# Performance work log

Hardware: AMD Instinct MI355X
Metric: run time of the kernel (lower is better)

## Reference

```python
import jax, jax.numpy as jnp
import numpy as np

LUT_VALS = np.array([-1.0, -0.5, -0.333333, -0.2, -0.142857, -0.090909, -0.076923,
                     0.0, 0.076923, 0.090909, 0.142857, 0.2, 0.333333, 0.5, 1.0],
                    dtype=np.float32)

B, S, IN, OUT = 4, 2048, 2048, 8192


def setup_inputs() -> dict:
    key = jax.random.key(0)
    kx, ki = jax.random.split(key)
    x = jax.random.normal(kx, (B, S, IN), dtype=jnp.float32)
    # uint8 LUT indices into the 15-entry primal grid (stored int32 for jax indexing)
    grid_indices = jax.random.randint(ki, (OUT, IN), 0, 15, dtype=jnp.int32)
    scale = jnp.float32(1.0)
    lut = jnp.asarray(LUT_VALS)
    return {"x": x, "grid_indices": grid_indices, "scale": scale, "lut": lut}


def reference(x, grid_indices, scale, lut):
    # Dequantize: gather LUT values by index, then scalar scale (GhostQuantFunction.forward)
    weights = lut[grid_indices] * scale          # [OUT, IN] fp32
    # F.linear(x, weights): y = x @ W^T
    return jnp.einsum('bsi,oi->bso', x, weights)
```

## Files before the change

### kernel.cpp

```cpp
#include <hip/hip_runtime.h>
#include <cstdint>

typedef short bf16x8 __attribute__((ext_vector_type(8)));
typedef unsigned short u16x8 __attribute__((ext_vector_type(8)));
typedef float f32x4 __attribute__((ext_vector_type(4)));
typedef __attribute__((address_space(3))) uint32_t lds_u32;
typedef const __attribute__((address_space(1))) uint32_t gbl_u32;

__device__ __forceinline__ unsigned short f2bf(float f) {
  union { float f; uint32_t u; } c; c.f = f;
  uint32_t u = c.u;
  return (unsigned short)((u + 0x7fffu + ((u >> 16) & 1u)) >> 16);
}

__global__ void cvt_x_kernel(const float* __restrict__ x,
                             unsigned short* __restrict__ y, long n) {
  long t = (long)blockIdx.x * blockDim.x + threadIdx.x;
  long base = t * 8;
  if (base >= n) return;
  const float4* p = (const float4*)(x + base);
  float4 f0 = p[0], f1 = p[1];
  u16x8 v;
  v[0] = f2bf(f0.x); v[1] = f2bf(f0.y); v[2] = f2bf(f0.z); v[3] = f2bf(f0.w);
  v[4] = f2bf(f1.x); v[5] = f2bf(f1.y); v[6] = f2bf(f1.z); v[7] = f2bf(f1.w);
  *(u16x8*)(y + base) = v;
}

__global__ void dequant_kernel(const int* __restrict__ idx,
                               const float* __restrict__ lut,
                               const float* __restrict__ scale,
                               unsigned short* __restrict__ w, long n) {
  __shared__ unsigned short slut[16];
  if (threadIdx.x < 15) slut[threadIdx.x] = f2bf(lut[threadIdx.x] * scale[0]);
  __syncthreads();
  long t = (long)blockIdx.x * blockDim.x + threadIdx.x;
  long base = t * 8;
  if (base >= n) return;
  const int4* p = (const int4*)(idx + base);
  int4 i0 = p[0], i1 = p[1];
  u16x8 v;
  v[0] = slut[i0.x]; v[1] = slut[i0.y]; v[2] = slut[i0.z]; v[3] = slut[i0.w];
  v[4] = slut[i1.x]; v[5] = slut[i1.y]; v[6] = slut[i1.z]; v[7] = slut[i1.w];
  *(u16x8*)(w + base) = v;
}


__device__ __forceinline__ void bar() {
  asm volatile("" ::: "memory");
  __builtin_amdgcn_s_barrier();
  asm volatile("" ::: "memory");
}

#define STAGE(D, R, G, KOFF)                                                  \
  do {                                                                        \
    lds_u32* dst_ = (lds_u32*)(&lds[0]) + (D) * 16384 + (R) * 4096 + t * 4;   \
    const unsigned short* s_ = (G) + (KOFF);                                  \
    __builtin_amdgcn_global_load_lds((gbl_u32*)(s_), dst_, 16, 0, 0);         \
    __builtin_amdgcn_global_load_lds((gbl_u32*)(s_ + (size_t)128 * 2048),     \
                                     dst_ + 2048, 16, 0, 0);                  \
  } while (0)

template <int D>
__device__ __forceinline__ void ktile(int T, unsigned short* lds,
                                      f32x4 (&acc)[8][4],
                                      const unsigned short* gA,
                                      const unsigned short* gB, int t,
                                      int aoff, int boff) {
  constexpr int NT = 32;
  const int c1 = (T + 1 < NT) ? (T + 1) : (NT - 1);
  const int c2 = (T + 2 < NT) ? (T + 2) : (NT - 1);
  const int k1 = c1 * 64, k2 = c2 * 64;

  const unsigned short* lA0 = &lds[D * 32768 + aoff];
  const unsigned short* lA1 = &lds[D * 32768 + 8192 + aoff];
  const unsigned short* lB0 = &lds[D * 32768 + 16384 + boff];
  const unsigned short* lB1 = &lds[D * 32768 + 24576 + boff];

  bf16x8 afr[8], b0, b1;

#pragma unroll
  for (int i = 0; i < 8; ++i) afr[i] = *(const bf16x8*)(lA0 + i * 512);
  b0 = *(const bf16x8*)(lB0);
  b1 = *(const bf16x8*)(lB0 + 512);
  STAGE(D ^ 1, 3, gB, k1 + 32);
  bar();
  __builtin_amdgcn_s_setprio(1);
#pragma unroll
  for (int i = 0; i < 8; ++i) {
    acc[i][0] = __builtin_amdgcn_mfma_f32_16x16x32_bf16(afr[i], b0, acc[i][0], 0, 0, 0);
    acc[i][1] = __builtin_amdgcn_mfma_f32_16x16x32_bf16(afr[i], b1, acc[i][1], 0, 0, 0);
  }
  __builtin_amdgcn_s_setprio(0);
  bar();

  b0 = *(const bf16x8*)(lB0 + 1024);
  b1 = *(const bf16x8*)(lB0 + 1536);
  STAGE(D ^ 1, 1, gA, k1 + 32);
  bar();
  __builtin_amdgcn_s_setprio(1);
#pragma unroll
  for (int i = 0; i < 8; ++i) {
    acc[i][2] = __builtin_amdgcn_mfma_f32_16x16x32_bf16(afr[i], b0, acc[i][2], 0, 0, 0);
    acc[i][3] = __builtin_amdgcn_mfma_f32_16x16x32_bf16(afr[i], b1, acc[i][3], 0, 0, 0);
  }
  __builtin_amdgcn_s_setprio(0);
  bar();

#pragma unroll
  for (int i = 0; i < 8; ++i) afr[i] = *(const bf16x8*)(lA1 + i * 512);
  b0 = *(const bf16x8*)(lB1);
  b1 = *(const bf16x8*)(lB1 + 512);
  STAGE(D, 0, gA, k2);
  bar();
  __builtin_amdgcn_s_setprio(1);
#pragma unroll
  for (int i = 0; i < 8; ++i) {
    acc[i][0] = __builtin_amdgcn_mfma_f32_16x16x32_bf16(afr[i], b0, acc[i][0], 0, 0, 0);
    acc[i][1] = __builtin_amdgcn_mfma_f32_16x16x32_bf16(afr[i], b1, acc[i][1], 0, 0, 0);
  }
  __builtin_amdgcn_s_setprio(0);
  bar();

  b0 = *(const bf16x8*)(lB1 + 1024);
  b1 = *(const bf16x8*)(lB1 + 1536);
  STAGE(D, 2, gB, k2);
  bar();
  __builtin_amdgcn_s_setprio(1);
#pragma unroll
  for (int i = 0; i < 8; ++i) {
    acc[i][2] = __builtin_amdgcn_mfma_f32_16x16x32_bf16(afr[i], b0, acc[i][2], 0, 0, 0);
    acc[i][3] = __builtin_amdgcn_mfma_f32_16x16x32_bf16(afr[i], b1, acc[i][3], 0, 0, 0);
  }
  __builtin_amdgcn_s_setprio(0);
  asm volatile("s_waitcnt vmcnt(4)" ::: "memory");
  bar();
}

__global__ __launch_bounds__(512, 2) void gemm_bt_256(
    const unsigned short* __restrict__ A,
    const unsigned short* __restrict__ B,
    float* __restrict__ C) {
  constexpr int K = 2048, N = 8192, NT = 32;
  __shared__ unsigned short lds[65536];

  const int t = threadIdx.x;
  const int l = t & 63;
  const int w = t >> 6;
  const int wm = w >> 2, wn = w & 3;

  const int bid = blockIdx.x;
  const int swz = (bid & 7) * 128 + (bid >> 3);
  const int bm = swz >> 5, bn = swz & 31;

  f32x4 acc[8][4] = {};

  const int lchunk = (t & 3) ^ ((t >> 3) & 3);
  const unsigned short* gA = A + (size_t)(bm * 256 + (t >> 2)) * K + lchunk * 8;
  const unsigned short* gB = B + (size_t)(bn * 256 + (t >> 2)) * K + lchunk * 8;

  const int sc8 = ((l >> 4) ^ ((l >> 1) & 3)) * 8;
  const int aoff = (wm * 128 + (l & 15)) * 32 + sc8;
  const int boff = (wn * 64 + (l & 15)) * 32 + sc8;

  STAGE(0, 0, gA, 0);
  STAGE(0, 2, gB, 0);
  STAGE(0, 3, gB, 32);
  STAGE(0, 1, gA, 32);
  STAGE(1, 0, gA, 64);
  STAGE(1, 2, gB, 64);
  asm volatile("s_waitcnt vmcnt(4)" ::: "memory");
  bar();

  for (int T = 0; T < NT; T += 2) {
    ktile<0>(T, lds, acc, gA, gB, t, aoff, boff);
    ktile<1>(T + 1, lds, acc, gA, gB, t, aoff, boff);
  }
  asm volatile("s_waitcnt vmcnt(0)" ::: "memory");

  float* Cp = C + (size_t)(bm * 256 + wm * 128 + ((l >> 4) << 2)) * N
              + bn * 256 + wn * 64 + (l & 15);
#pragma unroll
  for (int i = 0; i < 8; ++i)
#pragma unroll
    for (int j = 0; j < 4; ++j)
#pragma unroll
      for (int r = 0; r < 4; ++r)
        Cp[(size_t)(i * 16 + r) * N + j * 16] = acc[i][j][r];
}

extern "C" void kernel_launch(void* const* d_in, const int* in_sizes, int n_in,
                              void* d_out, int out_size, void* d_ws, size_t ws_size,
                              hipStream_t stream) {
  const float* x     = (const float*)d_in[0];
  const int*   gi    = (const int*)d_in[1];
  const float* scale = (const float*)d_in[2];
  const float* lut   = (const float*)d_in[3];
  float* out = (float*)d_out;

  const int M = 8192, N = 8192, K = 2048;
  unsigned short* xb = (unsigned short*)d_ws;
  unsigned short* wb = xb + (size_t)M * K;

  long nx = (long)M * K;
  long nw = (long)N * K;
  cvt_x_kernel<<<dim3((unsigned)(nx / (256 * 8))), dim3(256), 0, stream>>>(x, xb, nx);
  dequant_kernel<<<dim3((unsigned)(nw / (256 * 8))), dim3(256), 0, stream>>>(gi, lut, scale, wb, nw);

  gemm_bt_256<<<dim3((M / 256) * (N / 256)), dim3(512), 0, stream>>>(xb, wb, out);
}
```

Baseline: 601.2 us.

## Software-pipeline LDS fragment loads with double-buffered register fragments

Replaces the ktile template with a macro that keeps two sets of A/B register fragments. The next sub-tile's LDS reads are issued before the current MFMA block runs, so LDS read latency can hide behind matrix math. The vmcnt wait counts are retuned to fit the new schedule, and the first fragments are preloaded before the loop. The extra live fragment registers raise register pressure under the 512-thread, 2-block launch bound. Reading LDS earlier also depends on the barrier and wait counts exactly covering the asynchronous global-to-LDS writes.

```diff
diff --git a/kernel.cpp b/kernel.cpp
--- a/kernel.cpp
+++ b/kernel.cpp
@@ -60,81 +60,63 @@
                                      dst_ + 2048, 16, 0, 0);                  \
   } while (0)
 
-template <int D>
-__device__ __forceinline__ void ktile(int T, unsigned short* lds,
-                                      f32x4 (&acc)[8][4],
-                                      const unsigned short* gA,
-                                      const unsigned short* gB, int t,
-                                      int aoff, int boff) {
-  constexpr int NT = 32;
-  const int c1 = (T + 1 < NT) ? (T + 1) : (NT - 1);
-  const int c2 = (T + 2 < NT) ? (T + 2) : (NT - 1);
-  const int k1 = c1 * 64, k2 = c2 * 64;
+#define MFMA_PAIR(AF, B0_, B1_, J0, J1)                                       \
+  do {                                                                        \
+    __builtin_amdgcn_s_setprio(1);                                            \
+    _Pragma("unroll")                                                         \
+    for (int i = 0; i < 8; ++i) {                                             \
+      acc[i][J0] = __builtin_amdgcn_mfma_f32_16x16x32_bf16(AF[i], B0_, acc[i][J0], 0, 0, 0); \
+      acc[i][J1] = __builtin_amdgcn_mfma_f32_16x16x32_bf16(AF[i], B1_, acc[i][J1], 0, 0, 0); \
+    }                                                                         \
+    __builtin_amdgcn_s_setprio(0);                                            \
+  } while (0)
 
-  const unsigned short* lA0 = &lds[D * 32768 + aoff];
-  const unsigned short* lA1 = &lds[D * 32768 + 8192 + aoff];
-  const unsigned short* lB0 = &lds[D * 32768 + 16384 + boff];
-  const unsigned short* lB1 = &lds[D * 32768 + 24576 + boff];
-
-  bf16x8 afr[8], b0, b1;
-
-#pragma unroll
-  for (int i = 0; i < 8; ++i) afr[i] = *(const bf16x8*)(lA0 + i * 512);
-  b0 = *(const bf16x8*)(lB0);
-  b1 = *(const bf16x8*)(lB0 + 512);
-  STAGE(D ^ 1, 3, gB, k1 + 32);
-  bar();
-  __builtin_amdgcn_s_setprio(1);
-#pragma unroll
-  for (int i = 0; i < 8; ++i) {
-    acc[i][0] = __builtin_amdgcn_mfma_f32_16x16x32_bf16(afr[i], b0, acc[i][0], 0, 0, 0);
-    acc[i][1] = __builtin_amdgcn_mfma_f32_16x16x32_bf16(afr[i], b1, acc[i][1], 0, 0, 0);
-  }
-  __builtin_amdgcn_s_setprio(0);
-  bar();
-
-  b0 = *(const bf16x8*)(lB0 + 1024);
-  b1 = *(const bf16x8*)(lB0 + 1536);
-  STAGE(D ^ 1, 1, gA, k1 + 32);
-  bar();
-  __builtin_amdgcn_s_setprio(1);
-#pragma unroll
-  for (int i = 0; i < 8; ++i) {
-    acc[i][2] = __builtin_amdgcn_mfma_f32_16x16x32_bf16(afr[i], b0, acc[i][2], 0, 0, 0);
-    acc[i][3] = __builtin_amdgcn_mfma_f32_16x16x32_bf16(afr[i], b1, acc[i][3], 0, 0, 0);
-  }
-  __builtin_amdgcn_s_setprio(0);
-  bar();
-
-#pragma unroll
-  for (int i = 0; i < 8; ++i) afr[i] = *(const bf16x8*)(lA1 + i * 512);
-  b0 = *(const bf16x8*)(lB1);
-  b1 = *(const bf16x8*)(lB1 + 512);
-  STAGE(D, 0, gA, k2);
-  bar();
-  __builtin_amdgcn_s_setprio(1);
-#pragma unroll
-  for (int i = 0; i < 8; ++i) {
-    acc[i][0] = __builtin_amdgcn_mfma_f32_16x16x32_bf16(afr[i], b0, acc[i][0], 0, 0, 0);
-    acc[i][1] = __builtin_amdgcn_mfma_f32_16x16x32_bf16(afr[i], b1, acc[i][1], 0, 0, 0);
-  }
-  __builtin_amdgcn_s_setprio(0);
-  bar();
-
-  b0 = *(const bf16x8*)(lB1 + 1024);
-  b1 = *(const bf16x8*)(lB1 + 1536);
-  STAGE(D, 2, gB, k2);
-  bar();
-  __builtin_amdgcn_s_setprio(1);
-#pragma unroll
-  for (int i = 0; i < 8; ++i) {
-    acc[i][2] = __builtin_amdgcn_mfma_f32_16x16x32_bf16(afr[i], b0, acc[i][2], 0, 0, 0);
-    acc[i][3] = __builtin_amdgcn_mfma_f32_16x16x32_bf16(afr[i], b1, acc[i][3], 0, 0, 0);
-  }
-  __builtin_amdgcn_s_setprio(0);
-  asm volatile("s_waitcnt vmcnt(4)" ::: "memory");
-  bar();
-}
+#define KTILE(D_, T_)                                                         \
+  do {                                                                        \
+    const int c1 = ((T_) + 1 < NT) ? (T_) + 1 : (NT - 1);                     \
+    const int c2 = ((T_) + 2 < NT) ? (T_) + 2 : (NT - 1);                     \
+    const int k1 = c1 * 64, k2 = c2 * 64;                                     \
+    const unsigned short* lA1_  = &lds[(D_) * 32768 + 8192 + aoff];           \
+    const unsigned short* lB0_  = &lds[(D_) * 32768 + 16384 + boff];          \
+    const unsigned short* lB1_  = &lds[(D_) * 32768 + 24576 + boff];          \
+    const unsigned short* lA0n_ = &lds[((D_) ^ 1) * 32768 + aoff];            \
+    const unsigned short* lB0n_ = &lds[((D_) ^ 1) * 32768 + 16384 + boff];    \
+                  \
+    bA2 = *(const bf16x8*)(lB0_ + 1024);                                      \
+    bA3 = *(const bf16x8*)(lB0_ + 1536);                                      \
+    STAGE((D_) ^ 1, 3, gB, k1 + 32);                                          \
+    bar();                                                                    \
+    MFMA_PAIR(afrA, bA0, bA1, 0, 1);                                          \
+    bar();                                                                    \
+    \
+                                             \
+    asm volatile("s_waitcnt vmcnt(6)" ::: "memory");                          \
+    _Pragma("unroll")                                                         \
+    for (int i = 0; i < 8; ++i) afrB[i] = *(const bf16x8*)(lA1_ + i * 512);   \
+    bB0 = *(const bf16x8*)(lB1_);                                             \
+    bB1 = *(const bf16x8*)(lB1_ + 512);                                       \
+    STAGE((D_) ^ 1, 1, gA, k1 + 32);                                          \
+    bar();                                                                    \
+    MFMA_PAIR(afrA, bA2, bA3, 2, 3);                                          \
+    bar();                                                                    \
+                  \
+    bB2 = *(const bf16x8*)(lB1_ + 1024);                                      \
+    bB3 = *(const bf16x8*)(lB1_ + 1536);                                      \
+    STAGE((D_), 0, gA, k2);                                                   \
+    bar();                                                                    \
+    MFMA_PAIR(afrB, bB0, bB1, 0, 1);                                          \
+    bar();                                                                    \
+             \
+    asm volatile("s_waitcnt vmcnt(6)" ::: "memory");                          \
+    _Pragma("unroll")                                                         \
+    for (int i = 0; i < 8; ++i) afrA[i] = *(const bf16x8*)(lA0n_ + i * 512);  \
+    bA0 = *(const bf16x8*)(lB0n_);                                            \
+    bA1 = *(const bf16x8*)(lB0n_ + 512);                                      \
+    STAGE((D_), 2, gB, k2);                                                   \
+    bar();                                                                    \
+    MFMA_PAIR(afrB, bB2, bB3, 2, 3);                                          \
+    bar();                                                                    \
+  } while (0)
 
 __global__ __launch_bounds__(512, 2) void gemm_bt_256(
     const unsigned short* __restrict__ A,
@@ -162,18 +144,24 @@
   const int aoff = (wm * 128 + (l & 15)) * 32 + sc8;
   const int boff = (wn * 64 + (l & 15)) * 32 + sc8;
 
+  bf16x8 afrA[8], afrB[8], bA0, bA1, bA2, bA3, bB0, bB1, bB2, bB3;
+
   STAGE(0, 0, gA, 0);
   STAGE(0, 2, gB, 0);
   STAGE(0, 3, gB, 32);
   STAGE(0, 1, gA, 32);
   STAGE(1, 0, gA, 64);
   STAGE(1, 2, gB, 64);
-  asm volatile("s_waitcnt vmcnt(4)" ::: "memory");
+  asm volatile("s_waitcnt vmcnt(8)" ::: "memory");
   bar();
+#pragma unroll
+  for (int i = 0; i < 8; ++i) afrA[i] = *(const bf16x8*)(&lds[aoff] + i * 512);
+  bA0 = *(const bf16x8*)(&lds[16384 + boff]);
+  bA1 = *(const bf16x8*)(&lds[16384 + boff] + 512);
 
   for (int T = 0; T < NT; T += 2) {
-    ktile<0>(T, lds, acc, gA, gB, t, aoff, boff);
-    ktile<1>(T + 1, lds, acc, gA, gB, t, aoff, boff);
+    KTILE(0, T);
+    KTILE(1, T + 1);
   }
   asm volatile("s_waitcnt vmcnt(0)" ::: "memory");
 
```

Result: no change. 609.3 us (+1.3%).
